# Kernel optimization log

Measured on AMD Instinct MI355X. Metric: run time of the kernel, lower is better.

Reference implementation:

```python
import jax, jax.numpy as jnp
import numpy as np
from jax import lax

# ---- global config (G in the original repo) ----
S_BASE = 13
SCALES = (1.0, 2.0, 4.0)
B = 3
NUM_CLASSES = 80
# ---- loss hyperparams (module defaults) ----
LAMBDA_COORD = 1.0
LAMBDA_NOOBJ = 1.0
LAMBDA_OBJ = 1.0
LAMBDA_CLASS = 1.0
LAMBDA_PRIOR = 0.0
IOU_THRES = 0.7
EPOCH_PRIOR = 0
SCALE_COORD = True
NO_OBJ_V3 = True
EPS = 1e-6


def _yolo2bbox(t):
    """Yolo2BBoxSingle: [N,S,S,B,5] cell-relative (x,y,w,h,conf) -> absolute
    corner boxes (x1,y1,x2,y2,conf) normalized to [0,1]."""
    S = t.shape[1]
    g = jnp.arange(S, dtype=t.dtype)
    cx = (t[..., 0] + g[None, None, :, None]) / S  # col index -> x
    cy = (t[..., 1] + g[None, :, None, None]) / S  # row index -> y
    w, h = t[..., 2], t[..., 3]
    return jnp.stack([cx - w / 2, cy - h / 2, cx + w / 2, cy + h / 2, t[..., 4]], axis=-1)


def setup_inputs() -> dict:
    key = jax.random.key(0)
    k1, k2, k3 = jax.random.split(key, 3)
    N, S = 64, 52
    C = (5 + NUM_CLASSES) * B  # 255
    yhat = jax.random.uniform(k1, (N, S, S, C), dtype=jnp.float32, minval=0.01, maxval=1.0)
    y = jax.random.uniform(k2, (N, S, S, C), dtype=jnp.float32, minval=0.01, maxval=1.0)
    anchors = jax.random.uniform(k3, (len(SCALES), B, 2), dtype=jnp.float32, minval=0.05, maxval=0.9)
    return {"yhat": yhat, "y": y, "anchors": anchors, "epoch": 1}


def reference(yhat, y, anchors, epoch):
    N = yhat.shape[0]
    SR = y.shape[1]
    scale_idx = SCALES.index(SR / S_BASE)  # static python
    S = SR
    yhat = yhat.reshape(N, S, S, B, 5 + NUM_CLASSES)
    y = y.reshape(N, S, S, B, 5 + NUM_CLASSES)

    # ---- IoU between every predicted box and every gt box in a cell (no grad) ----
    hb = lax.stop_gradient(_yolo2bbox(yhat[..., 0:5]))  # [N,S,S,B,5]
    yb = lax.stop_gradient(_yolo2bbox(y[..., 0:5]))     # [N,S,S,B,5]
    a = hb[:, :, :, :, None, :]  # pred box axis 3   -> [N,S,S,B,1,5]
    b = yb[:, :, :, None, :, :]  # gt   box axis 4   -> [N,S,S,1,B,5]
    wi = jnp.maximum(jnp.minimum(a[..., 2], b[..., 2]) - jnp.maximum(a[..., 0], b[..., 0]), 0.0)
    hi = jnp.maximum(jnp.minimum(a[..., 3], b[..., 3]) - jnp.maximum(a[..., 1], b[..., 1]), 0.0)
    inter = wi * hi
    union = ((a[..., 2] - a[..., 0]) * (a[..., 3] - a[..., 1])
             + (b[..., 2] - b[..., 0]) * (b[..., 3] - b[..., 1]) - inter)
    iou = inter / (union + EPS)                       # [N,S,S,B_pred,B_gt]
    max_iou = iou.max(axis=4)                         # best gt IoU per predicted box
    no_obj_iou = (max_iou < IOU_THRES).astype(yhat.dtype)
    # best predicted box per gt box (argmax over pred axis after permute)
    idx = jnp.argmax(jnp.swapaxes(iou, 3, 4), axis=4)[..., None]  # [N,S,S,B,1] int

    anc = anchors[scale_idx]                          # [B,2]
    wh_hat = jnp.log(yhat[..., 2:4] / anc + EPS)
    wh_true = jnp.log(y[..., 2:4] / anc + EPS)

    yhat_res = jnp.take_along_axis(yhat, jnp.broadcast_to(idx, (N, S, S, B, 5 + NUM_CLASSES)), axis=3)
    wh_hat_res = jnp.take_along_axis(wh_hat, jnp.broadcast_to(idx, (N, S, S, B, 2)), axis=3)

    have_obj = lax.stop_gradient((y[..., 4] > 0).astype(yhat.dtype))
    sq = lambda p, t: (p - t) ** 2

    coord = (sq(yhat_res[..., 0:2], y[..., 0:2]) + sq(wh_hat_res, wh_true)).sum(-1) * have_obj * LAMBDA_COORD
    if SCALE_COORD:
        coord = coord * (2.0 - y[..., 2] * y[..., 3])
    coord_loss = coord.sum(axis=(1, 2, 3))

    class_loss = (sq(yhat_res[..., 5:], y[..., 5:]).sum(-1) * have_obj * LAMBDA_CLASS).sum(axis=(1, 2, 3))

    no_obj_t = jnp.zeros_like(y[..., 4]) if NO_OBJ_V3 else y[..., 4]
    no_obj_loss = (sq(yhat[..., 4], no_obj_t) * no_obj_iou * LAMBDA_NOOBJ).sum(axis=(1, 2, 3))

    obj_loss = (sq(yhat_res[..., 4], y[..., 4]) * have_obj * LAMBDA_OBJ).sum(axis=(1, 2, 3))

    if epoch < EPOCH_PRIOR:
        prior_loss = (sq(yhat[..., 2:4], anc).sum(axis=(3, 4)) * LAMBDA_PRIOR).sum(axis=(1, 2))
    else:
        prior_loss = jnp.zeros((1,), yhat.dtype)

    return coord_loss, class_loss, no_obj_loss, obj_loss, prior_loss
```

## Files before the change

kernel.cpp:

```cpp
#include <hip/hip_runtime.h>


constexpr int SD      = 52;
constexpr int S2CELLS = SD * SD;
constexpr int CH      = 255;
constexpr int CPB     = 16;
constexpr int BIMG    = 16;
constexpr int CHUNKS  = S2CELLS / CPB;
constexpr float EPSF  = 1e-6f;

__device__ __forceinline__ float flog(float x) {
    return __builtin_amdgcn_logf(x) * 0.69314718055994531f;
}
__device__ __forceinline__ float frcp(float x) {
    return __builtin_amdgcn_rcpf(x);
}
__device__ __forceinline__ float sel3(int s, float a, float b, float c) {
    return (s == 0) ? a : ((s == 1) ? b : c);
}

__global__ __launch_bounds__(256, 4) void yolo_loss_kernel(
    const float* __restrict__ yhat, const float* __restrict__ yt,
    const float* __restrict__ anchors, float* __restrict__ out, int N)
{
    __shared__ float red[4][4];

    const int tid  = threadIdx.x;
    const int wv   = tid >> 6;
    const int lane = tid & 63;
    const int grp  = lane >> 4;
    const int sub  = lane & 15;
    const int cellLocal = wv * 4 + grp;

    const int n   = blockIdx.x >> 4;
    const int blk = blockIdx.x & (BIMG - 1);

    const float aw0 = anchors[12], ah0 = anchors[13];
    const float aw1 = anchors[14], ah1 = anchors[15];
    const float aw2 = anchors[16], ah2 = anchors[17];
    const float rw0 = frcp(aw0), rh0 = frcp(ah0);
    const float rw1 = frcp(aw1), rh1 = frcp(ah1);
    const float rw2 = frcp(aw2), rh2 = frcp(ah2);
    const float invS = 1.0f / (float)SD;

    float acc_coord = 0.f, acc_class = 0.f, acc_noobj = 0.f, acc_obj = 0.f;

    const size_t imgBase = (size_t)n * S2CELLS * CH;

    for (int c = blk; c < CHUNKS; c += BIMG) {
        const int cellImg = c * CPB + cellLocal;
        const float* __restrict__ A = yhat + imgBase + (size_t)cellImg * CH;
        const float* __restrict__ T = yt   + imgBase + (size_t)cellImg * CH;

        float av[3][5], tv[3][5];
        float acv[3][5], tcv[3][5];
#pragma unroll
        for (int b = 0; b < 3; b++)
#pragma unroll
            for (int k = 0; k < 5; k++) {
                av[b][k] = A[b * 85 + k];
                tv[b][k] = T[b * 85 + k];
            }
#pragma unroll
        for (int b = 0; b < 3; b++)
#pragma unroll
            for (int k = 0; k < 5; k++) {
                int cc = b * 85 + 5 + sub + k * 16;
                acv[b][k] = A[cc];
                tcv[b][k] = T[cc];
            }

        const int irow = cellImg / SD;
        const int jcol = cellImg - irow * SD;
        const float jf = (float)jcol, if_ = (float)irow;

        float hx1[3], hx2[3], hy1[3], hy2[3], ha[3];
        float tx1[3], tx2[3], ty1[3], ty2[3], ta[3];
#pragma unroll
        for (int b = 0; b < 3; b++) {
            float w = av[b][2], h = av[b][3];
            float cx = (av[b][0] + jf) * invS, cy = (av[b][1] + if_) * invS;
            hx1[b] = cx - 0.5f * w; hx2[b] = cx + 0.5f * w;
            hy1[b] = cy - 0.5f * h; hy2[b] = cy + 0.5f * h;
            ha[b]  = (hx2[b] - hx1[b]) * (hy2[b] - hy1[b]);
        }
#pragma unroll
        for (int b = 0; b < 3; b++) {
            float w = tv[b][2], h = tv[b][3];
            float cx = (tv[b][0] + jf) * invS, cy = (tv[b][1] + if_) * invS;
            tx1[b] = cx - 0.5f * w; tx2[b] = cx + 0.5f * w;
            ty1[b] = cy - 0.5f * h; ty2[b] = cy + 0.5f * h;
            ta[b]  = (tx2[b] - tx1[b]) * (ty2[b] - ty1[b]);
        }

        float iou[3][3];
#pragma unroll
        for (int bp = 0; bp < 3; bp++)
#pragma unroll
            for (int bt = 0; bt < 3; bt++) {
                float wi = fminf(hx2[bp], tx2[bt]) - fmaxf(hx1[bp], tx1[bt]);
                wi = fmaxf(wi, 0.0f);
                float hi = fminf(hy2[bp], ty2[bt]) - fmaxf(hy1[bp], ty1[bt]);
                hi = fmaxf(hi, 0.0f);
                float inter = wi * hi;
                float uni   = ha[bp] + ta[bt] - inter;
                iou[bp][bt] = inter * frcp(uni + EPSF);
            }

#pragma unroll
        for (int bp = 0; bp < 3; bp++) {
            float m = fmaxf(fmaxf(iou[bp][0], iou[bp][1]), iou[bp][2]);
            acc_noobj += (m < 0.7f) ? av[bp][4] * av[bp][4] : 0.0f;
        }

        int sel[3];
#pragma unroll
        for (int bt = 0; bt < 3; bt++) {
            int s = 0; float v = iou[0][bt];
            if (iou[1][bt] > v) { v = iou[1][bt]; s = 1; }
            if (iou[2][bt] > v) { s = 2; }
            sel[bt] = s;
        }

        float ho[3];
#pragma unroll
        for (int bt = 0; bt < 3; bt++) {
            int sp = sel[bt];
            float hoo = (tv[bt][4] > 0.0f) ? 1.0f : 0.0f;
            ho[bt] = hoo;
            float phx = sel3(sp, av[0][0], av[1][0], av[2][0]);
            float phy = sel3(sp, av[0][1], av[1][1], av[2][1]);
            float phw = sel3(sp, av[0][2], av[1][2], av[2][2]);
            float phh = sel3(sp, av[0][3], av[1][3], av[2][3]);
            float phc = sel3(sp, av[0][4], av[1][4], av[2][4]);
            float rwp = sel3(sp, rw0, rw1, rw2);
            float rhp = sel3(sp, rh0, rh1, rh2);
            float rwt = (bt == 0) ? rw0 : ((bt == 1) ? rw1 : rw2);
            float rht = (bt == 0) ? rh0 : ((bt == 1) ? rh1 : rh2);
            float dx  = phx - tv[bt][0];
            float dy  = phy - tv[bt][1];
            float dlw = flog(phw * rwp + EPSF) - flog(tv[bt][2] * rwt + EPSF);
            float dlh = flog(phh * rhp + EPSF) - flog(tv[bt][3] * rht + EPSF);
            float csum = dx * dx + dy * dy + dlw * dlw + dlh * dlh;
            acc_coord += csum * hoo * (2.0f - tv[bt][2] * tv[bt][3]);
            float dcf = phc - tv[bt][4];
            acc_obj += dcf * dcf * hoo;
        }

#pragma unroll
        for (int bt = 0; bt < 3; bt++) {
            int sp = sel[bt];
            float s = 0.0f;
#pragma unroll
            for (int k = 0; k < 5; k++) {
                float pa = sel3(sp, acv[0][k], acv[1][k], acv[2][k]);
                float d  = pa - tcv[bt][k];
                s += d * d;
            }
            acc_class += s * ho[bt];
        }
    }

#pragma unroll
    for (int off = 1; off < 64; off <<= 1) {
        acc_coord += __shfl_xor(acc_coord, off, 64);
        acc_class += __shfl_xor(acc_class, off, 64);
        acc_noobj += __shfl_xor(acc_noobj, off, 64);
        acc_obj   += __shfl_xor(acc_obj,   off, 64);
    }
    if (lane == 0) {
        red[wv][0] = acc_coord; red[wv][1] = acc_class;
        red[wv][2] = acc_noobj; red[wv][3] = acc_obj;
    }
    __syncthreads();
    if (tid < 4) {
        float s = red[0][tid] + red[1][tid] + red[2][tid] + red[3][tid];
        if (tid != 1) s *= 0.0625f;
        atomicAdd(&out[tid * N + n], s);
    }
}

extern "C" void kernel_launch(void* const* d_in, const int* in_sizes, int n_in,
                              void* d_out, int out_size, void* d_ws, size_t ws_size,
                              hipStream_t stream) {
    const float* yhat = (const float*)d_in[0];
    const float* yv   = (const float*)d_in[1];
    const float* anc  = (const float*)d_in[2];
    float* out = (float*)d_out;

    const int N = in_sizes[0] / (S2CELLS * CH);

    hipMemsetAsync(d_out, 0, (size_t)out_size * sizeof(float), stream);

    dim3 grid(N * BIMG);
    yolo_loss_kernel<<<grid, 256, 0, stream>>>(yhat, yv, anc, out, N);
}
```

Before: 78.50 us.

## Vectorize per-lane loads with unaligned float4 and double blocks per image

Loads now use unaligned 4-wide vector reads: the first four box fields go in one float4 and the confidence in a separate scalar. Each of the 16 lanes in a cell group now reads its own 5 contiguous class channels instead of 5 channels strided by 16. That cuts the number of load instructions but makes each lane's accesses less coalesced across the wave. The number of blocks per image also doubles from 16 to 32, which halves the chunk iterations per block and raises parallelism.

Result: slower. 99.34 us (+26.6%).

```diff
diff --git a/kernel.cpp b/kernel.cpp
--- a/kernel.cpp
+++ b/kernel.cpp
@@ -5,9 +5,11 @@
 constexpr int S2CELLS = SD * SD;
 constexpr int CH      = 255;
 constexpr int CPB     = 16;
-constexpr int BIMG    = 16;
+constexpr int BIMG    = 32;
 constexpr int CHUNKS  = S2CELLS / CPB;
 constexpr float EPSF  = 1e-6f;
+
+typedef float f4u __attribute__((ext_vector_type(4), aligned(4)));
 
 __device__ __forceinline__ float flog(float x) {
     return __builtin_amdgcn_logf(x) * 0.69314718055994531f;
@@ -32,7 +34,7 @@
     const int sub  = lane & 15;
     const int cellLocal = wv * 4 + grp;
 
-    const int n   = blockIdx.x >> 4;
+    const int n   = blockIdx.x >> 5;
     const int blk = blockIdx.x & (BIMG - 1);
 
     const float aw0 = anchors[12], ah0 = anchors[13];
@@ -46,29 +48,28 @@
     float acc_coord = 0.f, acc_class = 0.f, acc_noobj = 0.f, acc_obj = 0.f;
 
     const size_t imgBase = (size_t)n * S2CELLS * CH;
+    const int clsOff = 5 + 5 * sub;
 
     for (int c = blk; c < CHUNKS; c += BIMG) {
         const int cellImg = c * CPB + cellLocal;
         const float* __restrict__ A = yhat + imgBase + (size_t)cellImg * CH;
         const float* __restrict__ T = yt   + imgBase + (size_t)cellImg * CH;
 
-        float av[3][5], tv[3][5];
-        float acv[3][5], tcv[3][5];
-#pragma unroll
-        for (int b = 0; b < 3; b++)
-#pragma unroll
-            for (int k = 0; k < 5; k++) {
-                av[b][k] = A[b * 85 + k];
-                tv[b][k] = T[b * 85 + k];
-            }
-#pragma unroll
-        for (int b = 0; b < 3; b++)
-#pragma unroll
-            for (int k = 0; k < 5; k++) {
-                int cc = b * 85 + 5 + sub + k * 16;
-                acv[b][k] = A[cc];
-                tcv[b][k] = T[cc];
-            }
+        f4u  abox[3], tbox[3];
+        float acf[3], tcf[3];
+        f4u  acl4[3], tcl4[3];
+        float acl1[3], tcl1[3];
+#pragma unroll
+        for (int b = 0; b < 3; b++) {
+            abox[b] = *reinterpret_cast<const f4u*>(A + b * 85);
+            tbox[b] = *reinterpret_cast<const f4u*>(T + b * 85);
+            acf[b]  = A[b * 85 + 4];
+            tcf[b]  = T[b * 85 + 4];
+            acl4[b] = *reinterpret_cast<const f4u*>(A + b * 85 + clsOff);
+            tcl4[b] = *reinterpret_cast<const f4u*>(T + b * 85 + clsOff);
+            acl1[b] = A[b * 85 + clsOff + 4];
+            tcl1[b] = T[b * 85 + clsOff + 4];
+        }
 
         const int irow = cellImg / SD;
         const int jcol = cellImg - irow * SD;
@@ -78,16 +79,16 @@
         float tx1[3], tx2[3], ty1[3], ty2[3], ta[3];
 #pragma unroll
         for (int b = 0; b < 3; b++) {
-            float w = av[b][2], h = av[b][3];
-            float cx = (av[b][0] + jf) * invS, cy = (av[b][1] + if_) * invS;
+            float w = abox[b].z, h = abox[b].w;
+            float cx = (abox[b].x + jf) * invS, cy = (abox[b].y + if_) * invS;
             hx1[b] = cx - 0.5f * w; hx2[b] = cx + 0.5f * w;
             hy1[b] = cy - 0.5f * h; hy2[b] = cy + 0.5f * h;
             ha[b]  = (hx2[b] - hx1[b]) * (hy2[b] - hy1[b]);
         }
 #pragma unroll
         for (int b = 0; b < 3; b++) {
-            float w = tv[b][2], h = tv[b][3];
-            float cx = (tv[b][0] + jf) * invS, cy = (tv[b][1] + if_) * invS;
+            float w = tbox[b].z, h = tbox[b].w;
+            float cx = (tbox[b].x + jf) * invS, cy = (tbox[b].y + if_) * invS;
             tx1[b] = cx - 0.5f * w; tx2[b] = cx + 0.5f * w;
             ty1[b] = cy - 0.5f * h; ty2[b] = cy + 0.5f * h;
             ta[b]  = (tx2[b] - tx1[b]) * (ty2[b] - ty1[b]);
@@ -110,7 +111,7 @@
 #pragma unroll
         for (int bp = 0; bp < 3; bp++) {
             float m = fmaxf(fmaxf(iou[bp][0], iou[bp][1]), iou[bp][2]);
-            acc_noobj += (m < 0.7f) ? av[bp][4] * av[bp][4] : 0.0f;
+            acc_noobj += (m < 0.7f) ? acf[bp] * acf[bp] : 0.0f;
         }
 
         int sel[3];
@@ -126,24 +127,24 @@
 #pragma unroll
         for (int bt = 0; bt < 3; bt++) {
             int sp = sel[bt];
-            float hoo = (tv[bt][4] > 0.0f) ? 1.0f : 0.0f;
+            float hoo = (tcf[bt] > 0.0f) ? 1.0f : 0.0f;
             ho[bt] = hoo;
-            float phx = sel3(sp, av[0][0], av[1][0], av[2][0]);
-            float phy = sel3(sp, av[0][1], av[1][1], av[2][1]);
-            float phw = sel3(sp, av[0][2], av[1][2], av[2][2]);
-            float phh = sel3(sp, av[0][3], av[1][3], av[2][3]);
-            float phc = sel3(sp, av[0][4], av[1][4], av[2][4]);
+            float phx = sel3(sp, abox[0].x, abox[1].x, abox[2].x);
+            float phy = sel3(sp, abox[0].y, abox[1].y, abox[2].y);
+            float phw = sel3(sp, abox[0].z, abox[1].z, abox[2].z);
+            float phh = sel3(sp, abox[0].w, abox[1].w, abox[2].w);
+            float phc = sel3(sp, acf[0],  acf[1],  acf[2]);
             float rwp = sel3(sp, rw0, rw1, rw2);
             float rhp = sel3(sp, rh0, rh1, rh2);
             float rwt = (bt == 0) ? rw0 : ((bt == 1) ? rw1 : rw2);
             float rht = (bt == 0) ? rh0 : ((bt == 1) ? rh1 : rh2);
-            float dx  = phx - tv[bt][0];
-            float dy  = phy - tv[bt][1];
-            float dlw = flog(phw * rwp + EPSF) - flog(tv[bt][2] * rwt + EPSF);
-            float dlh = flog(phh * rhp + EPSF) - flog(tv[bt][3] * rht + EPSF);
+            float dx  = phx - tbox[bt].x;
+            float dy  = phy - tbox[bt].y;
+            float dlw = flog(phw * rwp + EPSF) - flog(tbox[bt].z * rwt + EPSF);
+            float dlh = flog(phh * rhp + EPSF) - flog(tbox[bt].w * rht + EPSF);
             float csum = dx * dx + dy * dy + dlw * dlw + dlh * dlh;
-            acc_coord += csum * hoo * (2.0f - tv[bt][2] * tv[bt][3]);
-            float dcf = phc - tv[bt][4];
+            acc_coord += csum * hoo * (2.0f - tbox[bt].z * tbox[bt].w);
+            float dcf = phc - tcf[bt];
             acc_obj += dcf * dcf * hoo;
         }
 
@@ -152,9 +153,14 @@
             int sp = sel[bt];
             float s = 0.0f;
 #pragma unroll
-            for (int k = 0; k < 5; k++) {
-                float pa = sel3(sp, acv[0][k], acv[1][k], acv[2][k]);
-                float d  = pa - tcv[bt][k];
+            for (int k = 0; k < 4; k++) {
+                float pa = sel3(sp, acl4[0][k], acl4[1][k], acl4[2][k]);
+                float d  = pa - tcl4[bt][k];
+                s += d * d;
+            }
+            {
+                float pa = sel3(sp, acl1[0], acl1[1], acl1[2]);
+                float d  = pa - tcl1[bt];
                 s += d * d;
             }
             acc_class += s * ho[bt];
```
